# Kernel tuning notes

Measured on AMD Instinct MI355X. Metric: run time of the kernel, lower is better.

Reference implementation:

```python
import jax, jax.numpy as jnp
import numpy as np

N = 50000        # nodes
E = 800000       # directed edges (before self-loops)
F_IN = 128       # input node features
HID = 32         # hidden channels per head
HEADS = 4
NCLS = 8
EPS_BN = 1e-5
NEG_SLOPE = 0.2  # GATConv LeakyReLU default


def setup_inputs() -> dict:
    key = jax.random.key(0)
    ks = jax.random.split(key, 16)
    rn = lambda k, shape, s=0.1: jax.random.normal(k, shape, jnp.float32) * s
    inp = {}
    inp["x"] = jax.random.normal(ks[0], (N, F_IN), jnp.float32)
    inp["edge_index"] = jax.random.randint(ks[1], (2, E), 0, N, dtype=jnp.int32)
    # layer 0: F_IN -> HEADS*HID (concat)
    inp["W0"] = rn(ks[2], (F_IN, HEADS * HID))
    inp["as0"] = rn(ks[3], (HEADS, HID))
    inp["ad0"] = rn(ks[4], (HEADS, HID))
    inp["b0"] = jnp.zeros((HEADS * HID,), jnp.float32)
    inp["g0"] = jnp.ones((HEADS * HID,), jnp.float32)
    inp["bb0"] = jnp.zeros((HEADS * HID,), jnp.float32)
    inp["rm0"] = jnp.zeros((HEADS * HID,), jnp.float32)
    inp["rv0"] = jnp.ones((HEADS * HID,), jnp.float32)
    # layer 1: HEADS*HID -> HEADS*HID (concat)
    inp["W1"] = rn(ks[5], (HEADS * HID, HEADS * HID))
    inp["as1"] = rn(ks[6], (HEADS, HID))
    inp["ad1"] = rn(ks[7], (HEADS, HID))
    inp["b1"] = jnp.zeros((HEADS * HID,), jnp.float32)
    inp["g1"] = jnp.ones((HEADS * HID,), jnp.float32)
    inp["bb1"] = jnp.zeros((HEADS * HID,), jnp.float32)
    inp["rm1"] = jnp.zeros((HEADS * HID,), jnp.float32)
    inp["rv1"] = jnp.ones((HEADS * HID,), jnp.float32)
    # layer 2: HEADS*HID -> NCLS, heads=1, concat=False
    inp["W2"] = rn(ks[8], (HEADS * HID, NCLS))
    inp["as2"] = rn(ks[9], (1, NCLS))
    inp["ad2"] = rn(ks[10], (1, NCLS))
    inp["b2"] = jnp.zeros((NCLS,), jnp.float32)
    return inp


def gat_conv(x, src, dst, W, att_s, att_d, bias, H, C, concat):
    """PyG-style GATConv (eval mode, self-loops already appended to src/dst)."""
    n = x.shape[0]
    h = (x @ W).reshape(n, H, C)                       # [N,H,C]
    a_s = (h * att_s).sum(-1)                          # [N,H]
    a_d = (h * att_d).sum(-1)                          # [N,H]
    e = jax.nn.leaky_relu(a_s[src] + a_d[dst], NEG_SLOPE)  # [E,H]
    # numerically-stable segment softmax over incoming edges of each dst node
    m = jax.ops.segment_max(e, dst, num_segments=n)
    m = jnp.where(jnp.isfinite(m), m, 0.0)
    ex = jnp.exp(e - m[dst])
    den = jax.ops.segment_sum(ex, dst, num_segments=n)
    alpha = ex / (den[dst] + 1e-16)                    # [E,H]
    out = jax.ops.segment_sum(h[src] * alpha[:, :, None], dst, num_segments=n)  # [N,H,C]
    out = out.reshape(n, H * C) if concat else out.mean(axis=1)
    return out + bias


def bn_eval(x, g, b, rm, rv):
    return (x - rm) * jax.lax.rsqrt(rv + EPS_BN) * g + b


def reference(x, edge_index, W0, as0, ad0, b0, g0, bb0, rm0, rv0,
              W1, as1, ad1, b1, g1, bb1, rm1, rv1, W2, as2, ad2, b2):
    n = x.shape[0]
    loop = jnp.arange(n, dtype=edge_index.dtype)       # self-loops (PyG default)
    src = jnp.concatenate([edge_index[0], loop])
    dst = jnp.concatenate([edge_index[1], loop])
    h = gat_conv(x, src, dst, W0, as0, ad0, b0, HEADS, HID, True)
    h = jax.nn.elu(bn_eval(h, g0, bb0, rm0, rv0))
    h = gat_conv(h, src, dst, W1, as1, ad1, b1, HEADS, HID, True)
    h = jax.nn.elu(bn_eval(h, g1, bb1, rm1, rv1))
    h = gat_conv(h, src, dst, W2, as2, ad2, b2, 1, NCLS, False)
    return jax.nn.log_softmax(h, axis=1)
```

## Files before the change

kernel.cpp:

```cpp
#include <hip/hip_runtime.h>
#include <math.h>

#define N_NODES 50000
#define N_EDGES 800000
#define ET (N_EDGES + N_NODES)
#define FDIM 128
#define HEADS 4
#define HID 32
#define NCLS 8
#define NEG 0.2f
#define EPS_BN 1e-5f

#define BSH 6
#define NBUCK ((N_NODES + 63) >> BSH)
#define EPB 4096

typedef __attribute__((ext_vector_type(8))) short short8;
typedef __attribute__((ext_vector_type(4))) float f32x4;

__device__ __forceinline__ float lrelu(float e) { return e > 0.f ? e : NEG * e; }
__device__ __forceinline__ float bflo(unsigned u) { return __uint_as_float(u << 16); }
__device__ __forceinline__ float bfhi(unsigned u) { return __uint_as_float(u & 0xffff0000u); }
__device__ __forceinline__ unsigned f2bf(float f) {
    unsigned b = __float_as_uint(f);
    return (b + 0x7fffu + ((b >> 16) & 1u)) >> 16;
}

__device__ __forceinline__ void scan_bhist(const int* __restrict__ bhist,
                                           int* bloc, int* stmp) {
    int t = threadIdx.x;
    int idx = t * 4;
    int v0 = (idx     < NBUCK) ? bhist[idx]     : 0;
    int v1 = (idx + 1 < NBUCK) ? bhist[idx + 1] : 0;
    int v2 = (idx + 2 < NBUCK) ? bhist[idx + 2] : 0;
    int v3 = (idx + 3 < NBUCK) ? bhist[idx + 3] : 0;
    int sum = v0 + v1 + v2 + v3;
    stmp[t] = sum;
    __syncthreads();
    for (int off = 1; off < 256; off <<= 1) {
        int x = (t >= off) ? stmp[t - off] : 0;
        __syncthreads();
        stmp[t] += x;
        __syncthreads();
    }
    int run = stmp[t] - sum;
    if (idx     < NBUCK) bloc[idx]     = run; run += v0;
    if (idx + 1 < NBUCK) bloc[idx + 1] = run; run += v1;
    if (idx + 2 < NBUCK) bloc[idx + 2] = run; run += v2;
    if (idx + 3 < NBUCK) bloc[idx + 3] = run;
    __syncthreads();
}


#define CAST_B 3125
#define PACK_B 64
#define PB ((ET + EPB - 1) / EPB)

__global__ __launch_bounds__(256) void prep_hist(
        const float* __restrict__ x, unsigned short* __restrict__ xb,
        const float* __restrict__ W0, unsigned short* __restrict__ W0p,
        const float* __restrict__ W1, unsigned short* __restrict__ W1p,
        const int* __restrict__ ei, int* __restrict__ bhist) {
    __shared__ unsigned h[NBUCK];
    int b = blockIdx.x, tid = threadIdx.x;
    if (b < CAST_B) {
        int i = b * 256 + tid;
        const float4* p = (const float4*)x + (size_t)i * 2;
        float4 a = p[0], c = p[1];
        uint4 o;
        o.x = f2bf(a.x) | (f2bf(a.y) << 16);
        o.y = f2bf(a.z) | (f2bf(a.w) << 16);
        o.z = f2bf(c.x) | (f2bf(c.y) << 16);
        o.w = f2bf(c.z) | (f2bf(c.w) << 16);
        ((uint4*)xb)[i] = o;
    } else if (b < CAST_B + 2 * PACK_B) {
        int pb = b - CAST_B;
        const float* W = (pb < PACK_B) ? W0 : W1;
        unsigned short* Wp = (pb < PACK_B) ? W0p : W1p;
        int o = (pb & (PACK_B - 1)) * 256 + tid;
        int j = o & 7, lane = (o >> 3) & 63, kc = (o >> 9) & 3, t = o >> 11;
        int k = kc * 32 + ((lane >> 4) << 3) + j;
        int n = t * 16 + (lane & 15);
        Wp[o] = (unsigned short)f2bf(W[k * 128 + n]);
    } else {
        int blk = b - (CAST_B + 2 * PACK_B);
        int e0 = blk * EPB;
        for (int i = tid; i < NBUCK; i += 256) h[i] = 0;
        __syncthreads();
        #pragma unroll
        for (int k = 0; k < EPB / 256; k++) {
            int e = e0 + k * 256 + tid;
            if (e < ET) {
                int d = (e < N_EDGES) ? ei[N_EDGES + e] : (e - N_EDGES);
                atomicAdd(&h[d >> BSH], 1u);
            }
        }
        __syncthreads();
        for (int i = tid; i < NBUCK; i += 256)
            if (h[i]) atomicAdd(&bhist[i], (int)h[i]);
    }
}


__device__ __forceinline__ void gemm_attn_body(
        float* tiles, int gb,
        const unsigned short* __restrict__ Ab, const unsigned short* __restrict__ Wp,
        const float* __restrict__ att_s, const float* __restrict__ att_d,
        unsigned short* __restrict__ Hb, float* __restrict__ asn, float* __restrict__ adn,
        int M) {
    int tid = threadIdx.x;
    int wv = tid >> 6, lane = tid & 63;
    int base = gb * 64;
    int mrow = base + wv * 16 + (lane & 15);
    if (mrow >= M) mrow = M - 1;
    int koff = (lane >> 4) * 8;

    f32x4 acc[8];
    #pragma unroll
    for (int t = 0; t < 8; t++) acc[t] = (f32x4){0.f, 0.f, 0.f, 0.f};

    #pragma unroll
    for (int kc = 0; kc < 4; kc++) {
        short8 a = *(const short8*)(Ab + (size_t)mrow * 128 + kc * 32 + koff);
        #pragma unroll
        for (int t = 0; t < 8; t++) {
            short8 bfr = *(const short8*)(Wp + (((t * 4 + kc) * 64 + lane) << 3));
            acc[t] = __builtin_amdgcn_mfma_f32_16x16x32_bf16(a, bfr, acc[t], 0, 0, 0);
        }
    }

    int rbase = wv * 16 + (lane >> 4) * 4;
    int col = lane & 15;
    #pragma unroll
    for (int t = 0; t < 8; t++)
        #pragma unroll
        for (int r = 0; r < 4; r++)
            tiles[(rbase + r) * 132 + t * 16 + col] = acc[t][r];
    __syncthreads();

    #pragma unroll
    for (int it = 0; it < 4; it++) {
        int u = tid + it * 256;
        int rl = u >> 4, cg = u & 15;
        int row = base + rl;
        if (row < M) {
            const float* p = tiles + rl * 132 + cg * 8;
            float4 v0 = *(const float4*)(p);
            float4 v1 = *(const float4*)(p + 4);
            uint4 o;
            o.x = f2bf(v0.x) | (f2bf(v0.y) << 16);
            o.y = f2bf(v0.z) | (f2bf(v0.w) << 16);
            o.z = f2bf(v1.x) | (f2bf(v1.y) << 16);
            o.w = f2bf(v1.z) | (f2bf(v1.w) << 16);
            *(uint4*)(Hb + (size_t)row * 128 + cg * 8) = o;
        }
    }

    {
        int rl = tid >> 2, hd = tid & 3;
        int row = base + rl;
        if (row < M) {
            const float* hrow = tiles + rl * 132 + hd * 32;
            const float* as = att_s + hd * 32;
            const float* ad = att_d + hd * 32;
            float ps = 0.f, pd = 0.f;
            #pragma unroll
            for (int i = 0; i < 8; i++) {
                float4 hv = *(const float4*)(hrow + i * 4);
                float4 sv = *(const float4*)(as + i * 4);
                float4 dv = *(const float4*)(ad + i * 4);
                ps += hv.x * sv.x + hv.y * sv.y + hv.z * sv.z + hv.w * sv.w;
                pd += hv.x * dv.x + hv.y * dv.y + hv.z * dv.z + hv.w * dv.w;
            }
            asn[row * 4 + hd] = ps;
            adn[row * 4 + hd] = pd;
        }
    }
}


__global__ __launch_bounds__(256) void part_gemm(
        const int* __restrict__ ei, const int* __restrict__ bhist,
        int* __restrict__ bcur, int2* __restrict__ pairs,
        const unsigned short* __restrict__ Ab, const unsigned short* __restrict__ Wp,
        const float* __restrict__ att_s, const float* __restrict__ att_d,
        unsigned short* __restrict__ Hb, float* __restrict__ asn, float* __restrict__ adn,
        int M) {
    __shared__ float smem[64 * 132];
    int tid = threadIdx.x;
    if (blockIdx.x < PB) {
        unsigned* hist = (unsigned*)smem;
        unsigned* base = hist + NBUCK;
        int* bloc = (int*)(base + NBUCK);
        int* stmp = bloc + NBUCK;
        for (int i = tid; i < NBUCK; i += 256) hist[i] = 0;
        scan_bhist(bhist, bloc, stmp);
        int e0 = blockIdx.x * EPB;
        #pragma unroll
        for (int k = 0; k < EPB / 256; k++) {
            int e = e0 + k * 256 + tid;
            if (e < ET) {
                int d = (e < N_EDGES) ? ei[N_EDGES + e] : (e - N_EDGES);
                atomicAdd(&hist[d >> BSH], 1u);
            }
        }
        __syncthreads();
        for (int i = tid; i < NBUCK; i += 256) {
            unsigned h = hist[i];
            base[i] = h ? (unsigned)(bloc[i] + atomicAdd(&bcur[i], (int)h)) : 0u;
            hist[i] = 0;
        }
        __syncthreads();
        #pragma unroll
        for (int k = 0; k < EPB / 256; k++) {
            int e = e0 + k * 256 + tid;
            if (e < ET) {
                int s, d;
                if (e < N_EDGES) { s = ei[e]; d = ei[N_EDGES + e]; }
                else             { s = d = e - N_EDGES; }
                int bk = d >> BSH;
                unsigned lpos = atomicAdd(&hist[bk], 1u);
                pairs[base[bk] + lpos] = make_int2(s, d);
            }
        }
    } else {
        gemm_attn_body(smem, blockIdx.x - PB, Ab, Wp, att_s, att_d, Hb, asn, adn, M);
    }
}


__global__ __launch_bounds__(256) void group_bucket(const int2* __restrict__ pairs,
                                                    const int* __restrict__ bhist,
                                                    int* __restrict__ offs,
                                                    int* __restrict__ ssrc) {
    __shared__ int bloc[NBUCK];
    __shared__ int stmp[256];
    __shared__ int cnt[64];
    int b = blockIdx.x, tid = threadIdx.x;
    scan_bhist(bhist, bloc, stmp);
    int base = bloc[b];
    int end = (b + 1 < NBUCK) ? bloc[b + 1] : ET;
    int n0 = b << BSH;
    if (tid < 64) cnt[tid] = 0;
    __syncthreads();
    for (int i = base + tid; i < end; i += 256)
        atomicAdd(&cnt[pairs[i].y & 63], 1);
    __syncthreads();
    int v = (tid < 64) ? cnt[tid] : 0;
    stmp[tid] = v;
    __syncthreads();
    for (int off = 1; off < 64; off <<= 1) {
        int x = (tid >= off) ? stmp[tid - off] : 0;
        __syncthreads();
        stmp[tid] += x;
        __syncthreads();
    }
    int excl = stmp[tid] - v;
    if (tid < 64) {
        if (n0 + tid < N_NODES) offs[n0 + tid] = base + excl;
        cnt[tid] = excl;
    }
    __syncthreads();
    for (int i = base + tid; i < end; i += 256) {
        int2 p = pairs[i];
        int pos = atomicAdd(&cnt[p.y & 63], 1);
        ssrc[base + pos] = p.x;
    }
    if (b == 0 && tid == 0) offs[N_NODES] = ET;
}


#define AGB 16
#define NAGB (N_NODES / AGB)

__global__ __launch_bounds__(256) void agg_gemm1(
        const unsigned short* __restrict__ hb, const float* __restrict__ asn,
        const float* __restrict__ adn, const int* __restrict__ offs,
        const int* __restrict__ ssrc, const float* __restrict__ bias,
        const float* __restrict__ gamma, const float* __restrict__ beta,
        const float* __restrict__ rmean, const float* __restrict__ rvar,
        const unsigned short* __restrict__ Wp,
        const float* __restrict__ att_s, const float* __restrict__ att_d,
        unsigned short* __restrict__ Hb2, float* __restrict__ asn1,
        float* __restrict__ adn1) {
    __shared__ __attribute__((aligned(16))) unsigned short At[16][136];
    __shared__ __attribute__((aligned(16))) int2 sPair[4][4][72];
    float* ftile = (float*)&sPair[0][0][0];

    int tid = threadIdx.x;
    int wv = tid >> 6, lane = tid & 63;
    int hd = lane >> 4;
    const unsigned short* hlane = hb + 2 * lane;
    const int2* pp = &sPair[wv][hd][0];

    if (lane < 32) sPair[wv][lane >> 3][64 + (lane & 7)] = make_int2(0, 0);

    int c0 = lane * 2;
    float2 bi = *(const float2*)(bias + c0);
    float2 gm = *(const float2*)(gamma + c0);
    float2 bt = *(const float2*)(beta + c0);
    float2 rm = *(const float2*)(rmean + c0);
    float2 rv = *(const float2*)(rvar + c0);
    float sc0 = rsqrtf(rv.x + EPS_BN) * gm.x;
    float sc1 = rsqrtf(rv.y + EPS_BN) * gm.y;

    #pragma unroll 1
    for (int q = 0; q < 4; q++) {
        int lr = wv * 4 + q;
        int node = blockIdx.x * AGB + lr;
        int beg = offs[node], deg = offs[node + 1] - beg;
        float4 ad4 = *(const float4*)(adn + node * 4);
        float4 den4 = make_float4(0.f, 0.f, 0.f, 0.f);
        float acc0 = 0.f, acc1 = 0.f;

        auto phaseC = [&](int cnt) {
            int bound = (cnt + 7) & ~7;
            for (int i = 0; i < bound; i += 8) {
                int2 p0 = pp[i],     p1 = pp[i + 1], p2 = pp[i + 2], p3 = pp[i + 3];
                int2 p4 = pp[i + 4], p5 = pp[i + 5], p6 = pp[i + 6], p7 = pp[i + 7];
                unsigned u0 = *(const unsigned*)(hlane + (((unsigned)p0.x) << 7));
                unsigned u1 = *(const unsigned*)(hlane + (((unsigned)p1.x) << 7));
                unsigned u2 = *(const unsigned*)(hlane + (((unsigned)p2.x) << 7));
                unsigned u3 = *(const unsigned*)(hlane + (((unsigned)p3.x) << 7));
                unsigned u4 = *(const unsigned*)(hlane + (((unsigned)p4.x) << 7));
                unsigned u5 = *(const unsigned*)(hlane + (((unsigned)p5.x) << 7));
                unsigned u6 = *(const unsigned*)(hlane + (((unsigned)p6.x) << 7));
                unsigned u7 = *(const unsigned*)(hlane + (((unsigned)p7.x) << 7));
                acc0 += __int_as_float(p0.y) * bflo(u0); acc1 += __int_as_float(p0.y) * bfhi(u0);
                acc0 += __int_as_float(p1.y) * bflo(u1); acc1 += __int_as_float(p1.y) * bfhi(u1);
                acc0 += __int_as_float(p2.y) * bflo(u2); acc1 += __int_as_float(p2.y) * bfhi(u2);
                acc0 += __int_as_float(p3.y) * bflo(u3); acc1 += __int_as_float(p3.y) * bfhi(u3);
                acc0 += __int_as_float(p4.y) * bflo(u4); acc1 += __int_as_float(p4.y) * bfhi(u4);
                acc0 += __int_as_float(p5.y) * bflo(u5); acc1 += __int_as_float(p5.y) * bfhi(u5);
                acc0 += __int_as_float(p6.y) * bflo(u6); acc1 += __int_as_float(p6.y) * bfhi(u6);
                acc0 += __int_as_float(p7.y) * bflo(u7); acc1 += __int_as_float(p7.y) * bfhi(u7);
            }
        };

        for (int base0 = 0; base0 < deg; base0 += 64) {
            int j = base0 + lane;
            int s = 0;
            float4 w4 = make_float4(0.f, 0.f, 0.f, 0.f);
            if (j < deg) {
                s = ssrc[beg + j];
                float4 a = *(const float4*)(asn + s * 4);
                w4.x = __expf(lrelu(a.x + ad4.x));
                w4.y = __expf(lrelu(a.y + ad4.y));
                w4.z = __expf(lrelu(a.z + ad4.z));
                w4.w = __expf(lrelu(a.w + ad4.w));
                den4.x += w4.x; den4.y += w4.y; den4.z += w4.z; den4.w += w4.w;
            }
            sPair[wv][0][lane] = make_int2(s, __float_as_int(w4.x));
            sPair[wv][1][lane] = make_int2(s, __float_as_int(w4.y));
            sPair[wv][2][lane] = make_int2(s, __float_as_int(w4.z));
            sPair[wv][3][lane] = make_int2(s, __float_as_int(w4.w));
            int cnt = deg - base0; if (cnt > 64) cnt = 64;
            phaseC(cnt);
        }

        #pragma unroll
        for (int off = 32; off; off >>= 1) {
            den4.x += __shfl_xor(den4.x, off);
            den4.y += __shfl_xor(den4.y, off);
            den4.z += __shfl_xor(den4.z, off);
            den4.w += __shfl_xor(den4.w, off);
        }
        float den = (hd & 2) ? ((hd & 1) ? den4.w : den4.z)
                             : ((hd & 1) ? den4.y : den4.x);
        float inv = 1.f / (den + 1e-16f);

        float o0 = acc0 * inv + bi.x;
        float o1 = acc1 * inv + bi.y;
        o0 = (o0 - rm.x) * sc0 + bt.x;
        o1 = (o1 - rm.y) * sc1 + bt.y;
        o0 = (o0 > 0.f) ? o0 : expm1f(o0);
        o1 = (o1 > 0.f) ? o1 : expm1f(o1);
        *(unsigned*)&At[lr][c0] = f2bf(o0) | (f2bf(o1) << 16);
    }
    __syncthreads();

    int koff = hd * 8;
    int ar = lane & 15;
    f32x4 acc2[2];
    acc2[0] = (f32x4){0.f, 0.f, 0.f, 0.f};
    acc2[1] = (f32x4){0.f, 0.f, 0.f, 0.f};
    #pragma unroll
    for (int kc = 0; kc < 4; kc++) {
        short8 a = *(const short8*)&At[ar][kc * 32 + koff];
        #pragma unroll
        for (int ti = 0; ti < 2; ti++) {
            int t = wv * 2 + ti;
            short8 bfr = *(const short8*)(Wp + (((t * 4 + kc) * 64 + lane) << 3));
            acc2[ti] = __builtin_amdgcn_mfma_f32_16x16x32_bf16(a, bfr, acc2[ti], 0, 0, 0);
        }
    }
    __syncthreads();

    int rbase = hd * 4;
    int col = lane & 15;
    #pragma unroll
    for (int ti = 0; ti < 2; ti++) {
        int t = wv * 2 + ti;
        #pragma unroll
        for (int r = 0; r < 4; r++)
            ftile[(rbase + r) * 132 + t * 16 + col] = acc2[ti][r];
    }
    __syncthreads();

    {
        int rl = tid >> 4, cg = tid & 15;
        int row = blockIdx.x * AGB + rl;
        const float* p = ftile + rl * 132 + cg * 8;
        float4 v0 = *(const float4*)(p);
        float4 v1 = *(const float4*)(p + 4);
        uint4 o;
        o.x = f2bf(v0.x) | (f2bf(v0.y) << 16);
        o.y = f2bf(v0.z) | (f2bf(v0.w) << 16);
        o.z = f2bf(v1.x) | (f2bf(v1.y) << 16);
        o.w = f2bf(v1.z) | (f2bf(v1.w) << 16);
        *(uint4*)(Hb2 + (size_t)row * 128 + cg * 8) = o;
    }
    if (tid < 64) {
        int rl = tid >> 2, h2d = tid & 3;
        int row = blockIdx.x * AGB + rl;
        const float* hrow = ftile + rl * 132 + h2d * 32;
        const float* as = att_s + h2d * 32;
        const float* ad = att_d + h2d * 32;
        float ps = 0.f, pd = 0.f;
        #pragma unroll
        for (int i = 0; i < 8; i++) {
            float4 hv = *(const float4*)(hrow + i * 4);
            float4 sv = *(const float4*)(as + i * 4);
            float4 dv = *(const float4*)(ad + i * 4);
            ps += hv.x * sv.x + hv.y * sv.y + hv.z * sv.z + hv.w * sv.w;
            pd += hv.x * dv.x + hv.y * dv.y + hv.z * dv.z + hv.w * dv.w;
        }
        asn1[row * 4 + h2d] = ps;
        adn1[row * 4 + h2d] = pd;
    }
}


__global__ __launch_bounds__(256) void agg_mv2(
        const unsigned short* __restrict__ hb, const float* __restrict__ asn,
        const float* __restrict__ adn, const int* __restrict__ offs,
        const int* __restrict__ ssrc, const float* __restrict__ bias,
        const float* __restrict__ gamma, const float* __restrict__ beta,
        const float* __restrict__ rmean, const float* __restrict__ rvar,
        const float* __restrict__ W2, const float* __restrict__ as2,
        const float* __restrict__ ad2, float* __restrict__ h2,
        float* __restrict__ as2n, float* __restrict__ ad2n) {
    __shared__ int2 sPair[4][4][72];
    int wv = threadIdx.x >> 6;
    int node = blockIdx.x * 4 + wv;
    if (node >= N_NODES) return;
    int lane = threadIdx.x & 63;
    int hd = lane >> 4;
    int beg = offs[node], deg = offs[node + 1] - beg;
    float4 ad4 = *(const float4*)(adn + node * 4);

    if (lane < 32) sPair[wv][lane >> 3][64 + (lane & 7)] = make_int2(0, 0);

    float4 den4 = make_float4(0.f, 0.f, 0.f, 0.f);
    float acc0 = 0.f, acc1 = 0.f;
    const unsigned short* hlane = hb + 2 * lane;
    const int2* pp = &sPair[wv][hd][0];

    auto phaseC = [&](int cnt) {
        int bound = (cnt + 7) & ~7;
        for (int i = 0; i < bound; i += 8) {
            int2 p0 = pp[i],     p1 = pp[i + 1], p2 = pp[i + 2], p3 = pp[i + 3];
            int2 p4 = pp[i + 4], p5 = pp[i + 5], p6 = pp[i + 6], p7 = pp[i + 7];
            unsigned u0 = *(const unsigned*)(hlane + (((unsigned)p0.x) << 7));
            unsigned u1 = *(const unsigned*)(hlane + (((unsigned)p1.x) << 7));
            unsigned u2 = *(const unsigned*)(hlane + (((unsigned)p2.x) << 7));
            unsigned u3 = *(const unsigned*)(hlane + (((unsigned)p3.x) << 7));
            unsigned u4 = *(const unsigned*)(hlane + (((unsigned)p4.x) << 7));
            unsigned u5 = *(const unsigned*)(hlane + (((unsigned)p5.x) << 7));
            unsigned u6 = *(const unsigned*)(hlane + (((unsigned)p6.x) << 7));
            unsigned u7 = *(const unsigned*)(hlane + (((unsigned)p7.x) << 7));
            acc0 += __int_as_float(p0.y) * bflo(u0); acc1 += __int_as_float(p0.y) * bfhi(u0);
            acc0 += __int_as_float(p1.y) * bflo(u1); acc1 += __int_as_float(p1.y) * bfhi(u1);
            acc0 += __int_as_float(p2.y) * bflo(u2); acc1 += __int_as_float(p2.y) * bfhi(u2);
            acc0 += __int_as_float(p3.y) * bflo(u3); acc1 += __int_as_float(p3.y) * bfhi(u3);
            acc0 += __int_as_float(p4.y) * bflo(u4); acc1 += __int_as_float(p4.y) * bfhi(u4);
            acc0 += __int_as_float(p5.y) * bflo(u5); acc1 += __int_as_float(p5.y) * bfhi(u5);
            acc0 += __int_as_float(p6.y) * bflo(u6); acc1 += __int_as_float(p6.y) * bfhi(u6);
            acc0 += __int_as_float(p7.y) * bflo(u7); acc1 += __int_as_float(p7.y) * bfhi(u7);
        }
    };

    for (int base0 = 0; base0 < deg; base0 += 64) {
        int j = base0 + lane;
        int s = 0;
        float4 w4 = make_float4(0.f, 0.f, 0.f, 0.f);
        if (j < deg) {
            s = ssrc[beg + j];
            float4 a = *(const float4*)(asn + s * 4);
            w4.x = __expf(lrelu(a.x + ad4.x));
            w4.y = __expf(lrelu(a.y + ad4.y));
            w4.z = __expf(lrelu(a.z + ad4.z));
            w4.w = __expf(lrelu(a.w + ad4.w));
            den4.x += w4.x; den4.y += w4.y; den4.z += w4.z; den4.w += w4.w;
        }
        sPair[wv][0][lane] = make_int2(s, __float_as_int(w4.x));
        sPair[wv][1][lane] = make_int2(s, __float_as_int(w4.y));
        sPair[wv][2][lane] = make_int2(s, __float_as_int(w4.z));
        sPair[wv][3][lane] = make_int2(s, __float_as_int(w4.w));
        int cnt = deg - base0; if (cnt > 64) cnt = 64;
        phaseC(cnt);
    }

    #pragma unroll
    for (int off = 32; off; off >>= 1) {
        den4.x += __shfl_xor(den4.x, off);
        den4.y += __shfl_xor(den4.y, off);
        den4.z += __shfl_xor(den4.z, off);
        den4.w += __shfl_xor(den4.w, off);
    }
    float den = (hd & 2) ? ((hd & 1) ? den4.w : den4.z)
                         : ((hd & 1) ? den4.y : den4.x);
    float inv = 1.f / (den + 1e-16f);

    int c0 = lane * 2;
    float2 bi = *(const float2*)(bias + c0);
    float2 gm = *(const float2*)(gamma + c0);
    float2 bt = *(const float2*)(beta + c0);
    float2 rm = *(const float2*)(rmean + c0);
    float2 rv = *(const float2*)(rvar + c0);
    float o0 = acc0 * inv + bi.x;
    float o1 = acc1 * inv + bi.y;
    o0 = (o0 - rm.x) * rsqrtf(rv.x + EPS_BN) * gm.x + bt.x;
    o1 = (o1 - rm.y) * rsqrtf(rv.y + EPS_BN) * gm.y + bt.y;
    o0 = (o0 > 0.f) ? o0 : expm1f(o0);
    o1 = (o1 > 0.f) ? o1 : expm1f(o1);

    const float4* w2r = (const float4*)(W2 + c0 * 8);
    float4 wa0 = w2r[0], wa1 = w2r[1], wb0 = w2r[2], wb1 = w2r[3];
    float t8[8];
    t8[0] = o0 * wa0.x + o1 * wb0.x;
    t8[1] = o0 * wa0.y + o1 * wb0.y;
    t8[2] = o0 * wa0.z + o1 * wb0.z;
    t8[3] = o0 * wa0.w + o1 * wb0.w;
    t8[4] = o0 * wa1.x + o1 * wb1.x;
    t8[5] = o0 * wa1.y + o1 * wb1.y;
    t8[6] = o0 * wa1.z + o1 * wb1.z;
    t8[7] = o0 * wa1.w + o1 * wb1.w;
    #pragma unroll
    for (int off = 32; off; off >>= 1)
        #pragma unroll
        for (int c = 0; c < 8; c++) t8[c] += __shfl_xor(t8[c], off);
    if (lane == 0) {
        float ps = 0.f, pd = 0.f;
        #pragma unroll
        for (int c = 0; c < 8; c++) {
            h2[(size_t)node * 8 + c] = t8[c];
            ps += t8[c] * as2[c];
            pd += t8[c] * ad2[c];
        }
        as2n[node] = ps;
        ad2n[node] = pd;
    }
}


__global__ __launch_bounds__(256) void aggregate2(
        const float* __restrict__ h2, const float* __restrict__ asn,
        const float* __restrict__ adn, const int* __restrict__ offs,
        const int* __restrict__ ssrc, const float* __restrict__ b2,
        float* __restrict__ out) {
    __shared__ int2 sPair[4][64];
    int wv = threadIdx.x >> 6;
    int node = blockIdx.x * 4 + wv;
    if (node >= N_NODES) return;
    int lane = threadIdx.x & 63;
    int g = lane >> 3, c = lane & 7;
    int beg = offs[node], end = offs[node + 1];
    int deg = end - beg;
    float adv = adn[node];

    float den = 0.f, acc = 0.f;
    auto phaseC = [&](int cnt) {
        int nIt = (cnt + 15) >> 4;
        const int2* pp = &sPair[wv][0];
        for (int i = 0; i < nIt; i++) {
            int e = i * 16 + g;
            int2 p0 = pp[e];
            int2 p1 = pp[e + 8];
            acc += __int_as_float(p0.y) * h2[(((unsigned)p0.x) << 3) + c];
            acc += __int_as_float(p1.y) * h2[(((unsigned)p1.x) << 3) + c];
        }
    };

    for (int base = 0; base < deg; base += 64) {
        int j = base + lane;
        int s = 0; float w = 0.f;
        if (j < deg) {
            s = ssrc[beg + j];
            w = __expf(lrelu(asn[s] + adv));
            den += w;
        }
        sPair[wv][lane] = make_int2(s, __float_as_int(w));
        int cnt = deg - base; if (cnt > 64) cnt = 64;
        phaseC(cnt);
    }

    acc += __shfl_xor(acc, 8); acc += __shfl_xor(acc, 16); acc += __shfl_xor(acc, 32);
    #pragma unroll
    for (int off = 32; off; off >>= 1) den += __shfl_xor(den, off);

    float o = acc / (den + 1e-16f) + b2[c];
    float mx = o;
    mx = fmaxf(mx, __shfl_xor(mx, 1));
    mx = fmaxf(mx, __shfl_xor(mx, 2));
    mx = fmaxf(mx, __shfl_xor(mx, 4));
    float ex = __expf(o - mx);
    float sm = ex;
    sm += __shfl_xor(sm, 1); sm += __shfl_xor(sm, 2); sm += __shfl_xor(sm, 4);
    if (g == 0) out[(size_t)node * 8 + c] = o - mx - logf(sm);
}


extern "C" void kernel_launch(void* const* d_in, const int* in_sizes, int n_in,
                              void* d_out, int out_size, void* d_ws, size_t ws_size,
                              hipStream_t stream) {
    const float* x   = (const float*)d_in[0];
    const int*   ei  = (const int*)d_in[1];
    const float* W0  = (const float*)d_in[2];
    const float* as0 = (const float*)d_in[3];
    const float* ad0 = (const float*)d_in[4];
    const float* b0  = (const float*)d_in[5];
    const float* g0  = (const float*)d_in[6];
    const float* bb0 = (const float*)d_in[7];
    const float* rm0 = (const float*)d_in[8];
    const float* rv0 = (const float*)d_in[9];
    const float* W1  = (const float*)d_in[10];
    const float* as1 = (const float*)d_in[11];
    const float* ad1 = (const float*)d_in[12];
    const float* b1  = (const float*)d_in[13];
    const float* g1  = (const float*)d_in[14];
    const float* bb1 = (const float*)d_in[15];
    const float* rm1 = (const float*)d_in[16];
    const float* rv1 = (const float*)d_in[17];
    const float* W2  = (const float*)d_in[18];
    const float* as2 = (const float*)d_in[19];
    const float* ad2 = (const float*)d_in[20];
    const float* b2  = (const float*)d_in[21];
    float* out = (float*)d_out;

    char* w = (char*)d_ws;
    size_t off = 0;
    auto carve = [&](size_t bytes) {
        void* p = w + off;
        off += (bytes + 255) & ~(size_t)255;
        return p;
    };
    unsigned short* xb   = (unsigned short*)carve((size_t)N_NODES * 128 * 2);
    unsigned short* Hb   = (unsigned short*)carve((size_t)N_NODES * 128 * 2);
    unsigned short* Hb2  = (unsigned short*)carve((size_t)N_NODES * 128 * 2);
    unsigned short* W0p  = (unsigned short*)carve(16384 * 2);
    unsigned short* W1p  = (unsigned short*)carve(16384 * 2);
    int*   offs   = (int*)carve((size_t)(N_NODES + 1) * 4);
    int*   bhist  = (int*)carve((size_t)NBUCK * 2 * 4);
    int*   bcur   = bhist + NBUCK;
    int*   ssrc   = (int*)carve((size_t)ET * 4);
    int2*  pairs  = (int2*)carve((size_t)ET * 8);
    float* asn0   = (float*)carve((size_t)N_NODES * 4 * 4);
    float* adn0   = (float*)carve((size_t)N_NODES * 4 * 4);
    float* asn1   = (float*)carve((size_t)N_NODES * 4 * 4);
    float* adn1   = (float*)carve((size_t)N_NODES * 4 * 4);
    float* h2     = (float*)carve((size_t)N_NODES * 8 * 4);
    float* as2n   = (float*)carve((size_t)N_NODES * 4);
    float* ad2n   = (float*)carve((size_t)N_NODES * 4);
    (void)ws_size; (void)in_sizes; (void)n_in; (void)out_size;

    const int GB = (N_NODES + 63) / 64;

    hipMemsetAsync(bhist, 0, (size_t)NBUCK * 2 * 4, stream);
    prep_hist<<<CAST_B + 2 * PACK_B + PB, 256, 0, stream>>>(x, xb, W0, W0p, W1, W1p, ei, bhist);
    part_gemm<<<PB + GB, 256, 0, stream>>>(ei, bhist, bcur, pairs,
                                           xb, W0p, as0, ad0, Hb, asn0, adn0, N_NODES);
    group_bucket<<<NBUCK, 256, 0, stream>>>(pairs, bhist, offs, ssrc);
    agg_gemm1<<<NAGB, 256, 0, stream>>>(Hb, asn0, adn0, offs, ssrc,
                                        b0, g0, bb0, rm0, rv0,
                                        W1p, as1, ad1, Hb2, asn1, adn1);
    agg_mv2<<<(N_NODES + 3) / 4, 256, 0, stream>>>(Hb2, asn1, adn1, offs, ssrc,
                                                   b1, g1, bb1, rm1, rv1,
                                                   W2, as2, ad2, h2, as2n, ad2n);
    aggregate2<<<(N_NODES + 3) / 4, 256, 0, stream>>>(h2, as2n, ad2n, offs, ssrc, b2, out);
}
```

Before: 279.7 us.

## Vectorize edge gathers: 16-byte row loads with multiple edges per wavefront

The aggregation loops in agg_gemm1, agg_mv2 and aggregate2 are reorganized so each lane loads 16 bytes of a source row (8 bf16 or 4 floats) instead of 4 bytes. Several edges are now handled in parallel across lane groups, and partial sums are combined with cross-lane shuffles afterwards. This is meant to cut the number of gather instructions and serial iterations per edge on the memory-bound neighbour aggregation. In exchange it needs more accumulator registers and extra shuffle reductions, and in aggregate2 padded work grows for low-degree nodes because chunks are rounded up to 32.

```diff
diff --git a/kernel.cpp b/kernel.cpp
--- a/kernel.cpp
+++ b/kernel.cpp
@@ -289,20 +289,24 @@
 
     int tid = threadIdx.x;
     int wv = tid >> 6, lane = tid & 63;
-    int hd = lane >> 4;
-    const unsigned short* hlane = hb + 2 * lane;
-    const int2* pp = &sPair[wv][hd][0];
-
-    if (lane < 32) sPair[wv][lane >> 3][64 + (lane & 7)] = make_int2(0, 0);
-
-    int c0 = lane * 2;
-    float2 bi = *(const float2*)(bias + c0);
-    float2 gm = *(const float2*)(gamma + c0);
-    float2 bt = *(const float2*)(beta + c0);
-    float2 rm = *(const float2*)(rmean + c0);
-    float2 rv = *(const float2*)(rvar + c0);
-    float sc0 = rsqrtf(rv.x + EPS_BN) * gm.x;
-    float sc1 = rsqrtf(rv.y + EPS_BN) * gm.y;
+    int g = lane >> 4, sl = lane & 15;
+    int hda = sl >> 2;
+    const unsigned short* hsl = hb + (sl << 3);
+    const int2* pph = &sPair[wv][hda][0];
+    int c0 = sl * 8;
+
+    float4 bi0 = *(const float4*)(bias + c0),  bi1 = *(const float4*)(bias + c0 + 4);
+    float4 gm0 = *(const float4*)(gamma + c0), gm1 = *(const float4*)(gamma + c0 + 4);
+    float4 bt0 = *(const float4*)(beta + c0),  bt1 = *(const float4*)(beta + c0 + 4);
+    float4 rm0v = *(const float4*)(rmean + c0), rm1v = *(const float4*)(rmean + c0 + 4);
+    float4 rv0v = *(const float4*)(rvar + c0),  rv1v = *(const float4*)(rvar + c0 + 4);
+    float sc[8] = { rsqrtf(rv0v.x + EPS_BN) * gm0.x, rsqrtf(rv0v.y + EPS_BN) * gm0.y,
+                    rsqrtf(rv0v.z + EPS_BN) * gm0.z, rsqrtf(rv0v.w + EPS_BN) * gm0.w,
+                    rsqrtf(rv1v.x + EPS_BN) * gm1.x, rsqrtf(rv1v.y + EPS_BN) * gm1.y,
+                    rsqrtf(rv1v.z + EPS_BN) * gm1.z, rsqrtf(rv1v.w + EPS_BN) * gm1.w };
+    float bia[8] = { bi0.x, bi0.y, bi0.z, bi0.w, bi1.x, bi1.y, bi1.z, bi1.w };
+    float btv[8] = { bt0.x, bt0.y, bt0.z, bt0.w, bt1.x, bt1.y, bt1.z, bt1.w };
+    float rmv[8] = { rm0v.x, rm0v.y, rm0v.z, rm0v.w, rm1v.x, rm1v.y, rm1v.z, rm1v.w };
 
     #pragma unroll 1
     for (int q = 0; q < 4; q++) {
@@ -311,31 +315,7 @@
         int beg = offs[node], deg = offs[node + 1] - beg;
         float4 ad4 = *(const float4*)(adn + node * 4);
         float4 den4 = make_float4(0.f, 0.f, 0.f, 0.f);
-        float acc0 = 0.f, acc1 = 0.f;
-
-        auto phaseC = [&](int cnt) {
-            int bound = (cnt + 7) & ~7;
-            for (int i = 0; i < bound; i += 8) {
-                int2 p0 = pp[i],     p1 = pp[i + 1], p2 = pp[i + 2], p3 = pp[i + 3];
-                int2 p4 = pp[i + 4], p5 = pp[i + 5], p6 = pp[i + 6], p7 = pp[i + 7];
-                unsigned u0 = *(const unsigned*)(hlane + (((unsigned)p0.x) << 7));
-                unsigned u1 = *(const unsigned*)(hlane + (((unsigned)p1.x) << 7));
-                unsigned u2 = *(const unsigned*)(hlane + (((unsigned)p2.x) << 7));
-                unsigned u3 = *(const unsigned*)(hlane + (((unsigned)p3.x) << 7));
-                unsigned u4 = *(const unsigned*)(hlane + (((unsigned)p4.x) << 7));
-                unsigned u5 = *(const unsigned*)(hlane + (((unsigned)p5.x) << 7));
-                unsigned u6 = *(const unsigned*)(hlane + (((unsigned)p6.x) << 7));
-                unsigned u7 = *(const unsigned*)(hlane + (((unsigned)p7.x) << 7));
-                acc0 += __int_as_float(p0.y) * bflo(u0); acc1 += __int_as_float(p0.y) * bfhi(u0);
-                acc0 += __int_as_float(p1.y) * bflo(u1); acc1 += __int_as_float(p1.y) * bfhi(u1);
-                acc0 += __int_as_float(p2.y) * bflo(u2); acc1 += __int_as_float(p2.y) * bfhi(u2);
-                acc0 += __int_as_float(p3.y) * bflo(u3); acc1 += __int_as_float(p3.y) * bfhi(u3);
-                acc0 += __int_as_float(p4.y) * bflo(u4); acc1 += __int_as_float(p4.y) * bfhi(u4);
-                acc0 += __int_as_float(p5.y) * bflo(u5); acc1 += __int_as_float(p5.y) * bfhi(u5);
-                acc0 += __int_as_float(p6.y) * bflo(u6); acc1 += __int_as_float(p6.y) * bfhi(u6);
-                acc0 += __int_as_float(p7.y) * bflo(u7); acc1 += __int_as_float(p7.y) * bfhi(u7);
-            }
-        };
+        float acc[8] = {0.f, 0.f, 0.f, 0.f, 0.f, 0.f, 0.f, 0.f};
 
         for (int base0 = 0; base0 < deg; base0 += 64) {
             int j = base0 + lane;
@@ -355,9 +335,28 @@
             sPair[wv][2][lane] = make_int2(s, __float_as_int(w4.z));
             sPair[wv][3][lane] = make_int2(s, __float_as_int(w4.w));
             int cnt = deg - base0; if (cnt > 64) cnt = 64;
-            phaseC(cnt);
-        }
-
+            int bound = (cnt + 7) & ~7;
+            for (int i = 0; i < bound; i += 8) {
+                int2 pa = pph[i + g], pb = pph[i + 4 + g];
+                uint4 ua = *(const uint4*)(hsl + (((unsigned)pa.x) << 7));
+                uint4 ub = *(const uint4*)(hsl + (((unsigned)pb.x) << 7));
+                float wa = __int_as_float(pa.y), wb = __int_as_float(pb.y);
+                acc[0] += wa * bflo(ua.x); acc[1] += wa * bfhi(ua.x);
+                acc[2] += wa * bflo(ua.y); acc[3] += wa * bfhi(ua.y);
+                acc[4] += wa * bflo(ua.z); acc[5] += wa * bfhi(ua.z);
+                acc[6] += wa * bflo(ua.w); acc[7] += wa * bfhi(ua.w);
+                acc[0] += wb * bflo(ub.x); acc[1] += wb * bfhi(ub.x);
+                acc[2] += wb * bflo(ub.y); acc[3] += wb * bfhi(ub.y);
+                acc[4] += wb * bflo(ub.z); acc[5] += wb * bfhi(ub.z);
+                acc[6] += wb * bflo(ub.w); acc[7] += wb * bfhi(ub.w);
+            }
+        }
+
+        #pragma unroll
+        for (int c = 0; c < 8; c++) {
+            acc[c] += __shfl_xor(acc[c], 16);
+            acc[c] += __shfl_xor(acc[c], 32);
+        }
         #pragma unroll
         for (int off = 32; off; off >>= 1) {
             den4.x += __shfl_xor(den4.x, off);
@@ -365,21 +364,26 @@
             den4.z += __shfl_xor(den4.z, off);
             den4.w += __shfl_xor(den4.w, off);
         }
-        float den = (hd & 2) ? ((hd & 1) ? den4.w : den4.z)
-                             : ((hd & 1) ? den4.y : den4.x);
+        float den = (hda & 2) ? ((hda & 1) ? den4.w : den4.z)
+                              : ((hda & 1) ? den4.y : den4.x);
         float inv = 1.f / (den + 1e-16f);
 
-        float o0 = acc0 * inv + bi.x;
-        float o1 = acc1 * inv + bi.y;
-        o0 = (o0 - rm.x) * sc0 + bt.x;
-        o1 = (o1 - rm.y) * sc1 + bt.y;
-        o0 = (o0 > 0.f) ? o0 : expm1f(o0);
-        o1 = (o1 > 0.f) ? o1 : expm1f(o1);
-        *(unsigned*)&At[lr][c0] = f2bf(o0) | (f2bf(o1) << 16);
-    }
-    __syncthreads();
-
-    int koff = hd * 8;
+        unsigned dw[4];
+        #pragma unroll
+        for (int k = 0; k < 4; k++) {
+            float e0 = acc[2 * k] * inv + bia[2 * k];
+            float e1 = acc[2 * k + 1] * inv + bia[2 * k + 1];
+            e0 = (e0 - rmv[2 * k]) * sc[2 * k] + btv[2 * k];
+            e1 = (e1 - rmv[2 * k + 1]) * sc[2 * k + 1] + btv[2 * k + 1];
+            e0 = (e0 > 0.f) ? e0 : expm1f(e0);
+            e1 = (e1 > 0.f) ? e1 : expm1f(e1);
+            dw[k] = f2bf(e0) | (f2bf(e1) << 16);
+        }
+        if (g == 0) *(uint4*)&At[lr][c0] = make_uint4(dw[0], dw[1], dw[2], dw[3]);
+    }
+    __syncthreads();
+
+    int koff = (lane >> 4) * 8;
     int ar = lane & 15;
     f32x4 acc2[2];
     acc2[0] = (f32x4){0.f, 0.f, 0.f, 0.f};
@@ -396,7 +400,7 @@
     }
     __syncthreads();
 
-    int rbase = hd * 4;
+    int rbase = (lane >> 4) * 4;
     int col = lane & 15;
     #pragma unroll
     for (int ti = 0; ti < 2; ti++) {
@@ -455,40 +459,15 @@
     int node = blockIdx.x * 4 + wv;
     if (node >= N_NODES) return;
     int lane = threadIdx.x & 63;
-    int hd = lane >> 4;
+    int g = lane >> 4, sl = lane & 15;
+    int hda = sl >> 2;
     int beg = offs[node], deg = offs[node + 1] - beg;
     float4 ad4 = *(const float4*)(adn + node * 4);
 
-    if (lane < 32) sPair[wv][lane >> 3][64 + (lane & 7)] = make_int2(0, 0);
-
     float4 den4 = make_float4(0.f, 0.f, 0.f, 0.f);
-    float acc0 = 0.f, acc1 = 0.f;
-    const unsigned short* hlane = hb + 2 * lane;
-    const int2* pp = &sPair[wv][hd][0];
-
-    auto phaseC = [&](int cnt) {
-        int bound = (cnt + 7) & ~7;
-        for (int i = 0; i < bound; i += 8) {
-            int2 p0 = pp[i],     p1 = pp[i + 1], p2 = pp[i + 2], p3 = pp[i + 3];
-            int2 p4 = pp[i + 4], p5 = pp[i + 5], p6 = pp[i + 6], p7 = pp[i + 7];
-            unsigned u0 = *(const unsigned*)(hlane + (((unsigned)p0.x) << 7));
-            unsigned u1 = *(const unsigned*)(hlane + (((unsigned)p1.x) << 7));
-            unsigned u2 = *(const unsigned*)(hlane + (((unsigned)p2.x) << 7));
-            unsigned u3 = *(const unsigned*)(hlane + (((unsigned)p3.x) << 7));
-            unsigned u4 = *(const unsigned*)(hlane + (((unsigned)p4.x) << 7));
-            unsigned u5 = *(const unsigned*)(hlane + (((unsigned)p5.x) << 7));
-            unsigned u6 = *(const unsigned*)(hlane + (((unsigned)p6.x) << 7));
-            unsigned u7 = *(const unsigned*)(hlane + (((unsigned)p7.x) << 7));
-            acc0 += __int_as_float(p0.y) * bflo(u0); acc1 += __int_as_float(p0.y) * bfhi(u0);
-            acc0 += __int_as_float(p1.y) * bflo(u1); acc1 += __int_as_float(p1.y) * bfhi(u1);
-            acc0 += __int_as_float(p2.y) * bflo(u2); acc1 += __int_as_float(p2.y) * bfhi(u2);
-            acc0 += __int_as_float(p3.y) * bflo(u3); acc1 += __int_as_float(p3.y) * bfhi(u3);
-            acc0 += __int_as_float(p4.y) * bflo(u4); acc1 += __int_as_float(p4.y) * bfhi(u4);
-            acc0 += __int_as_float(p5.y) * bflo(u5); acc1 += __int_as_float(p5.y) * bfhi(u5);
-            acc0 += __int_as_float(p6.y) * bflo(u6); acc1 += __int_as_float(p6.y) * bfhi(u6);
-            acc0 += __int_as_float(p7.y) * bflo(u7); acc1 += __int_as_float(p7.y) * bfhi(u7);
-        }
-    };
+    float acc[8] = {0.f, 0.f, 0.f, 0.f, 0.f, 0.f, 0.f, 0.f};
+    const unsigned short* hsl = hb + (sl << 3);
+    const int2* pph = &sPair[wv][hda][0];
 
     for (int base0 = 0; base0 < deg; base0 += 64) {
         int j = base0 + lane;
@@ -508,9 +487,28 @@
         sPair[wv][2][lane] = make_int2(s, __float_as_int(w4.z));
         sPair[wv][3][lane] = make_int2(s, __float_as_int(w4.w));
         int cnt = deg - base0; if (cnt > 64) cnt = 64;
-        phaseC(cnt);
-    }
-
+        int bound = (cnt + 7) & ~7;
+        for (int i = 0; i < bound; i += 8) {
+            int2 pa = pph[i + g], pb = pph[i + 4 + g];
+            uint4 ua = *(const uint4*)(hsl + (((unsigned)pa.x) << 7));
+            uint4 ub = *(const uint4*)(hsl + (((unsigned)pb.x) << 7));
+            float wa = __int_as_float(pa.y), wb = __int_as_float(pb.y);
+            acc[0] += wa * bflo(ua.x); acc[1] += wa * bfhi(ua.x);
+            acc[2] += wa * bflo(ua.y); acc[3] += wa * bfhi(ua.y);
+            acc[4] += wa * bflo(ua.z); acc[5] += wa * bfhi(ua.z);
+            acc[6] += wa * bflo(ua.w); acc[7] += wa * bfhi(ua.w);
+            acc[0] += wb * bflo(ub.x); acc[1] += wb * bfhi(ub.x);
+            acc[2] += wb * bflo(ub.y); acc[3] += wb * bfhi(ub.y);
+            acc[4] += wb * bflo(ub.z); acc[5] += wb * bfhi(ub.z);
+            acc[6] += wb * bflo(ub.w); acc[7] += wb * bfhi(ub.w);
+        }
+    }
+
+    #pragma unroll
+    for (int c = 0; c < 8; c++) {
+        acc[c] += __shfl_xor(acc[c], 16);
+        acc[c] += __shfl_xor(acc[c], 32);
+    }
     #pragma unroll
     for (int off = 32; off; off >>= 1) {
         den4.x += __shfl_xor(den4.x, off);
@@ -518,38 +516,47 @@
         den4.z += __shfl_xor(den4.z, off);
         den4.w += __shfl_xor(den4.w, off);
     }
-    float den = (hd & 2) ? ((hd & 1) ? den4.w : den4.z)
-                         : ((hd & 1) ? den4.y : den4.x);
+    float den = (hda & 2) ? ((hda & 1) ? den4.w : den4.z)
+                          : ((hda & 1) ? den4.y : den4.x);
     float inv = 1.f / (den + 1e-16f);
 
-    int c0 = lane * 2;
-    float2 bi = *(const float2*)(bias + c0);
-    float2 gm = *(const float2*)(gamma + c0);
-    float2 bt = *(const float2*)(beta + c0);
-    float2 rm = *(const float2*)(rmean + c0);
-    float2 rv = *(const float2*)(rvar + c0);
-    float o0 = acc0 * inv + bi.x;
-    float o1 = acc1 * inv + bi.y;
-    o0 = (o0 - rm.x) * rsqrtf(rv.x + EPS_BN) * gm.x + bt.x;
-    o1 = (o1 - rm.y) * rsqrtf(rv.y + EPS_BN) * gm.y + bt.y;
-    o0 = (o0 > 0.f) ? o0 : expm1f(o0);
-    o1 = (o1 > 0.f) ? o1 : expm1f(o1);
-
-    const float4* w2r = (const float4*)(W2 + c0 * 8);
-    float4 wa0 = w2r[0], wa1 = w2r[1], wb0 = w2r[2], wb1 = w2r[3];
-    float t8[8];
-    t8[0] = o0 * wa0.x + o1 * wb0.x;
-    t8[1] = o0 * wa0.y + o1 * wb0.y;
-    t8[2] = o0 * wa0.z + o1 * wb0.z;
-    t8[3] = o0 * wa0.w + o1 * wb0.w;
-    t8[4] = o0 * wa1.x + o1 * wb1.x;
-    t8[5] = o0 * wa1.y + o1 * wb1.y;
-    t8[6] = o0 * wa1.z + o1 * wb1.z;
-    t8[7] = o0 * wa1.w + o1 * wb1.w;
-    #pragma unroll
-    for (int off = 32; off; off >>= 1)
-        #pragma unroll
-        for (int c = 0; c < 8; c++) t8[c] += __shfl_xor(t8[c], off);
+    int c0 = sl * 8;
+    float4 bi0 = *(const float4*)(bias + c0),  bi1 = *(const float4*)(bias + c0 + 4);
+    float4 gm0 = *(const float4*)(gamma + c0), gm1 = *(const float4*)(gamma + c0 + 4);
+    float4 bt0 = *(const float4*)(beta + c0),  bt1 = *(const float4*)(beta + c0 + 4);
+    float4 rm0v = *(const float4*)(rmean + c0), rm1v = *(const float4*)(rmean + c0 + 4);
+    float4 rv0v = *(const float4*)(rvar + c0),  rv1v = *(const float4*)(rvar + c0 + 4);
+    float bia[8] = { bi0.x, bi0.y, bi0.z, bi0.w, bi1.x, bi1.y, bi1.z, bi1.w };
+    float gmv[8] = { gm0.x, gm0.y, gm0.z, gm0.w, gm1.x, gm1.y, gm1.z, gm1.w };
+    float btv[8] = { bt0.x, bt0.y, bt0.z, bt0.w, bt1.x, bt1.y, bt1.z, bt1.w };
+    float rmv[8] = { rm0v.x, rm0v.y, rm0v.z, rm0v.w, rm1v.x, rm1v.y, rm1v.z, rm1v.w };
+    float rvv[8] = { rv0v.x, rv0v.y, rv0v.z, rv0v.w, rv1v.x, rv1v.y, rv1v.z, rv1v.w };
+
+    float o[8];
+    #pragma unroll
+    for (int k = 0; k < 8; k++) {
+        float e = acc[k] * inv + bia[k];
+        e = (e - rmv[k]) * rsqrtf(rvv[k] + EPS_BN) * gmv[k] + btv[k];
+        o[k] = (e > 0.f) ? e : expm1f(e);
+    }
+
+    float t8[8] = {0.f, 0.f, 0.f, 0.f, 0.f, 0.f, 0.f, 0.f};
+    #pragma unroll
+    for (int k = 0; k < 8; k++) {
+        const float4* wr = (const float4*)(W2 + (size_t)(c0 + k) * 8);
+        float4 wlo = wr[0], whi = wr[1];
+        t8[0] += o[k] * wlo.x; t8[1] += o[k] * wlo.y;
+        t8[2] += o[k] * wlo.z; t8[3] += o[k] * wlo.w;
+        t8[4] += o[k] * whi.x; t8[5] += o[k] * whi.y;
+        t8[6] += o[k] * whi.z; t8[7] += o[k] * whi.w;
+    }
+    #pragma unroll
+    for (int c = 0; c < 8; c++) {
+        t8[c] += __shfl_xor(t8[c], 1);
+        t8[c] += __shfl_xor(t8[c], 2);
+        t8[c] += __shfl_xor(t8[c], 4);
+        t8[c] += __shfl_xor(t8[c], 8);
+    }
     if (lane == 0) {
         float ps = 0.f, pd = 0.f;
         #pragma unroll
@@ -574,23 +581,14 @@
     int node = blockIdx.x * 4 + wv;
     if (node >= N_NODES) return;
     int lane = threadIdx.x & 63;
-    int g = lane >> 3, c = lane & 7;
-    int beg = offs[node], end = offs[node + 1];
-    int deg = end - beg;
+    int grp = lane >> 1, sub = lane & 1;
+    int beg = offs[node], deg = offs[node + 1] - beg;
     float adv = adn[node];
 
-    float den = 0.f, acc = 0.f;
-    auto phaseC = [&](int cnt) {
-        int nIt = (cnt + 15) >> 4;
-        const int2* pp = &sPair[wv][0];
-        for (int i = 0; i < nIt; i++) {
-            int e = i * 16 + g;
-            int2 p0 = pp[e];
-            int2 p1 = pp[e + 8];
-            acc += __int_as_float(p0.y) * h2[(((unsigned)p0.x) << 3) + c];
-            acc += __int_as_float(p1.y) * h2[(((unsigned)p1.x) << 3) + c];
-        }
-    };
+    float den = 0.f;
+    float acc[4] = {0.f, 0.f, 0.f, 0.f};
+    const int2* pp = &sPair[wv][0];
+    const float* hsub = h2 + (sub << 2);
 
     for (int base = 0; base < deg; base += 64) {
         int j = base + lane;
@@ -602,22 +600,42 @@
         }
         sPair[wv][lane] = make_int2(s, __float_as_int(w));
         int cnt = deg - base; if (cnt > 64) cnt = 64;
-        phaseC(cnt);
-    }
-
-    acc += __shfl_xor(acc, 8); acc += __shfl_xor(acc, 16); acc += __shfl_xor(acc, 32);
+        int bound = (cnt + 31) & ~31;
+        for (int i = 0; i < bound; i += 32) {
+            int2 pr = pp[i + grp];
+            float wgt = __int_as_float(pr.y);
+            float4 v = *(const float4*)(hsub + (((unsigned)pr.x) << 3));
+            acc[0] += wgt * v.x; acc[1] += wgt * v.y;
+            acc[2] += wgt * v.z; acc[3] += wgt * v.w;
+        }
+    }
+
+    #pragma unroll
+    for (int c = 0; c < 4; c++) {
+        acc[c] += __shfl_xor(acc[c], 2);
+        acc[c] += __shfl_xor(acc[c], 4);
+        acc[c] += __shfl_xor(acc[c], 8);
+        acc[c] += __shfl_xor(acc[c], 16);
+        acc[c] += __shfl_xor(acc[c], 32);
+    }
     #pragma unroll
     for (int off = 32; off; off >>= 1) den += __shfl_xor(den, off);
-
-    float o = acc / (den + 1e-16f) + b2[c];
-    float mx = o;
+    float inv = 1.f / (den + 1e-16f);
+
+    float4 bv = *(const float4*)(b2 + (sub << 2));
+    float o0 = acc[0] * inv + bv.x;
+    float o1 = acc[1] * inv + bv.y;
+    float o2 = acc[2] * inv + bv.z;
+    float o3 = acc[3] * inv + bv.w;
+    float mx = fmaxf(fmaxf(o0, o1), fmaxf(o2, o3));
     mx = fmaxf(mx, __shfl_xor(mx, 1));
-    mx = fmaxf(mx, __shfl_xor(mx, 2));
-    mx = fmaxf(mx, __shfl_xor(mx, 4));
-    float ex = __expf(o - mx);
-    float sm = ex;
-    sm += __shfl_xor(sm, 1); sm += __shfl_xor(sm, 2); sm += __shfl_xor(sm, 4);
-    if (g == 0) out[(size_t)node * 8 + c] = o - mx - logf(sm);
+    float sm = __expf(o0 - mx) + __expf(o1 - mx) + __expf(o2 - mx) + __expf(o3 - mx);
+    sm += __shfl_xor(sm, 1);
+    if (lane < 2) {
+        float ls = logf(sm);
+        float4 ov = make_float4(o0 - mx - ls, o1 - mx - ls, o2 - mx - ls, o3 - mx - ls);
+        *(float4*)(out + (size_t)node * 8 + (sub << 2)) = ov;
+    }
 }
 
 
```

After: 367.8 us. 31.5% more time.

## Precompute per-edge attention weights in separate edge-parallel passes

Applied to the files above, without the earlier changes.

Computes exp(leaky_relu(a_s[src]+a_d[dst])) per sorted edge in dedicated passes: fused into group_bucket for layer 0, and in new edge_w/edge_w2k kernels for layers 1 and 2. The aggregation kernels then read contiguous precomputed weights instead of gathering source attention scores and evaluating exp. The aim is to shorten latency-bound gathers inside the aggregation loop, at the cost of two extra kernel launches, an extra sorted-dst array, and writing and re-reading a per-edge weight buffer.

```diff
diff --git a/kernel.cpp b/kernel.cpp
--- a/kernel.cpp
+++ b/kernel.cpp
@@ -232,7 +232,11 @@
 __global__ __launch_bounds__(256) void group_bucket(const int2* __restrict__ pairs,
                                                     const int* __restrict__ bhist,
                                                     int* __restrict__ offs,
-                                                    int* __restrict__ ssrc) {
+                                                    int* __restrict__ ssrc,
+                                                    int* __restrict__ sdst,
+                                                    const float* __restrict__ asn0,
+                                                    const float* __restrict__ adn0,
+                                                    float* __restrict__ ew0) {
     __shared__ int bloc[NBUCK];
     __shared__ int stmp[256];
     __shared__ int cnt[64];
@@ -264,9 +268,46 @@
     for (int i = base + tid; i < end; i += 256) {
         int2 p = pairs[i];
         int pos = atomicAdd(&cnt[p.y & 63], 1);
-        ssrc[base + pos] = p.x;
+        int e = base + pos;
+        ssrc[e] = p.x;
+        sdst[e] = p.y;
+        float4 a = *(const float4*)(asn0 + p.x * 4);
+        float4 d = *(const float4*)(adn0 + p.y * 4);
+        float4 w;
+        w.x = __expf(lrelu(a.x + d.x));
+        w.y = __expf(lrelu(a.y + d.y));
+        w.z = __expf(lrelu(a.z + d.z));
+        w.w = __expf(lrelu(a.w + d.w));
+        *(float4*)(ew0 + (size_t)e * 4) = w;
     }
     if (b == 0 && tid == 0) offs[N_NODES] = ET;
+}
+
+
+__global__ __launch_bounds__(256) void edge_w(
+        const int* __restrict__ ssrc, const int* __restrict__ sdst,
+        const float* __restrict__ asn, const float* __restrict__ adn,
+        float* __restrict__ ew) {
+    int e = blockIdx.x * 256 + threadIdx.x;
+    if (e >= ET) return;
+    int s = ssrc[e], d = sdst[e];
+    float4 a = *(const float4*)(asn + s * 4);
+    float4 b = *(const float4*)(adn + d * 4);
+    float4 w;
+    w.x = __expf(lrelu(a.x + b.x));
+    w.y = __expf(lrelu(a.y + b.y));
+    w.z = __expf(lrelu(a.z + b.z));
+    w.w = __expf(lrelu(a.w + b.w));
+    *(float4*)(ew + (size_t)e * 4) = w;
+}
+
+__global__ __launch_bounds__(256) void edge_w2k(
+        const int* __restrict__ ssrc, const int* __restrict__ sdst,
+        const float* __restrict__ asn, const float* __restrict__ adn,
+        float* __restrict__ ew) {
+    int e = blockIdx.x * 256 + threadIdx.x;
+    if (e >= ET) return;
+    ew[e] = __expf(lrelu(asn[ssrc[e]] + adn[sdst[e]]));
 }
 
 
@@ -274,12 +315,11 @@
 #define NAGB (N_NODES / AGB)
 
 __global__ __launch_bounds__(256) void agg_gemm1(
-        const unsigned short* __restrict__ hb, const float* __restrict__ asn,
-        const float* __restrict__ adn, const int* __restrict__ offs,
-        const int* __restrict__ ssrc, const float* __restrict__ bias,
-        const float* __restrict__ gamma, const float* __restrict__ beta,
-        const float* __restrict__ rmean, const float* __restrict__ rvar,
-        const unsigned short* __restrict__ Wp,
+        const unsigned short* __restrict__ hb, const float* __restrict__ ew,
+        const int* __restrict__ offs, const int* __restrict__ ssrc,
+        const float* __restrict__ bias, const float* __restrict__ gamma,
+        const float* __restrict__ beta, const float* __restrict__ rmean,
+        const float* __restrict__ rvar, const unsigned short* __restrict__ Wp,
         const float* __restrict__ att_s, const float* __restrict__ att_d,
         unsigned short* __restrict__ Hb2, float* __restrict__ asn1,
         float* __restrict__ adn1) {
@@ -309,7 +349,6 @@
         int lr = wv * 4 + q;
         int node = blockIdx.x * AGB + lr;
         int beg = offs[node], deg = offs[node + 1] - beg;
-        float4 ad4 = *(const float4*)(adn + node * 4);
         float4 den4 = make_float4(0.f, 0.f, 0.f, 0.f);
         float acc0 = 0.f, acc1 = 0.f;
 
@@ -343,11 +382,7 @@
             float4 w4 = make_float4(0.f, 0.f, 0.f, 0.f);
             if (j < deg) {
                 s = ssrc[beg + j];
-                float4 a = *(const float4*)(asn + s * 4);
-                w4.x = __expf(lrelu(a.x + ad4.x));
-                w4.y = __expf(lrelu(a.y + ad4.y));
-                w4.z = __expf(lrelu(a.z + ad4.z));
-                w4.w = __expf(lrelu(a.w + ad4.w));
+                w4 = *(const float4*)(ew + (size_t)(beg + j) * 4);
                 den4.x += w4.x; den4.y += w4.y; den4.z += w4.z; den4.w += w4.w;
             }
             sPair[wv][0][lane] = make_int2(s, __float_as_int(w4.x));
@@ -442,14 +477,13 @@
 
 
 __global__ __launch_bounds__(256) void agg_mv2(
-        const unsigned short* __restrict__ hb, const float* __restrict__ asn,
-        const float* __restrict__ adn, const int* __restrict__ offs,
-        const int* __restrict__ ssrc, const float* __restrict__ bias,
-        const float* __restrict__ gamma, const float* __restrict__ beta,
-        const float* __restrict__ rmean, const float* __restrict__ rvar,
-        const float* __restrict__ W2, const float* __restrict__ as2,
-        const float* __restrict__ ad2, float* __restrict__ h2,
-        float* __restrict__ as2n, float* __restrict__ ad2n) {
+        const unsigned short* __restrict__ hb, const float* __restrict__ ew,
+        const int* __restrict__ offs, const int* __restrict__ ssrc,
+        const float* __restrict__ bias, const float* __restrict__ gamma,
+        const float* __restrict__ beta, const float* __restrict__ rmean,
+        const float* __restrict__ rvar, const float* __restrict__ W2,
+        const float* __restrict__ as2, const float* __restrict__ ad2,
+        float* __restrict__ h2, float* __restrict__ as2n, float* __restrict__ ad2n) {
     __shared__ int2 sPair[4][4][72];
     int wv = threadIdx.x >> 6;
     int node = blockIdx.x * 4 + wv;
@@ -457,7 +491,6 @@
     int lane = threadIdx.x & 63;
     int hd = lane >> 4;
     int beg = offs[node], deg = offs[node + 1] - beg;
-    float4 ad4 = *(const float4*)(adn + node * 4);
 
     if (lane < 32) sPair[wv][lane >> 3][64 + (lane & 7)] = make_int2(0, 0);
 
@@ -496,11 +529,7 @@
         float4 w4 = make_float4(0.f, 0.f, 0.f, 0.f);
         if (j < deg) {
             s = ssrc[beg + j];
-            float4 a = *(const float4*)(asn + s * 4);
-            w4.x = __expf(lrelu(a.x + ad4.x));
-            w4.y = __expf(lrelu(a.y + ad4.y));
-            w4.z = __expf(lrelu(a.z + ad4.z));
-            w4.w = __expf(lrelu(a.w + ad4.w));
+            w4 = *(const float4*)(ew + (size_t)(beg + j) * 4);
             den4.x += w4.x; den4.y += w4.y; den4.z += w4.z; den4.w += w4.w;
         }
         sPair[wv][0][lane] = make_int2(s, __float_as_int(w4.x));
@@ -565,10 +594,9 @@
 
 
 __global__ __launch_bounds__(256) void aggregate2(
-        const float* __restrict__ h2, const float* __restrict__ asn,
-        const float* __restrict__ adn, const int* __restrict__ offs,
-        const int* __restrict__ ssrc, const float* __restrict__ b2,
-        float* __restrict__ out) {
+        const float* __restrict__ h2, const float* __restrict__ ew2,
+        const int* __restrict__ offs, const int* __restrict__ ssrc,
+        const float* __restrict__ b2, float* __restrict__ out) {
     __shared__ int2 sPair[4][64];
     int wv = threadIdx.x >> 6;
     int node = blockIdx.x * 4 + wv;
@@ -577,7 +605,6 @@
     int g = lane >> 3, c = lane & 7;
     int beg = offs[node], end = offs[node + 1];
     int deg = end - beg;
-    float adv = adn[node];
 
     float den = 0.f, acc = 0.f;
     auto phaseC = [&](int cnt) {
@@ -597,7 +624,7 @@
         int s = 0; float w = 0.f;
         if (j < deg) {
             s = ssrc[beg + j];
-            w = __expf(lrelu(asn[s] + adv));
+            w = ew2[beg + j];
             den += w;
         }
         sPair[wv][lane] = make_int2(s, __float_as_int(w));
@@ -664,6 +691,8 @@
     int*   bhist  = (int*)carve((size_t)NBUCK * 2 * 4);
     int*   bcur   = bhist + NBUCK;
     int*   ssrc   = (int*)carve((size_t)ET * 4);
+    int*   sdst   = (int*)carve((size_t)ET * 4);
+    float* ewf    = (float*)carve((size_t)ET * 4 * 4);
     int2*  pairs  = (int2*)carve((size_t)ET * 8);
     float* asn0   = (float*)carve((size_t)N_NODES * 4 * 4);
     float* adn0   = (float*)carve((size_t)N_NODES * 4 * 4);
@@ -675,17 +704,21 @@
     (void)ws_size; (void)in_sizes; (void)n_in; (void)out_size;
 
     const int GB = (N_NODES + 63) / 64;
+    const int EB = (ET + 255) / 256;
 
     hipMemsetAsync(bhist, 0, (size_t)NBUCK * 2 * 4, stream);
     prep_hist<<<CAST_B + 2 * PACK_B + PB, 256, 0, stream>>>(x, xb, W0, W0p, W1, W1p, ei, bhist);
     part_gemm<<<PB + GB, 256, 0, stream>>>(ei, bhist, bcur, pairs,
                                            xb, W0p, as0, ad0, Hb, asn0, adn0, N_NODES);
-    group_bucket<<<NBUCK, 256, 0, stream>>>(pairs, bhist, offs, ssrc);
-    agg_gemm1<<<NAGB, 256, 0, stream>>>(Hb, asn0, adn0, offs, ssrc,
+    group_bucket<<<NBUCK, 256, 0, stream>>>(pairs, bhist, offs, ssrc, sdst,
+                                            asn0, adn0, ewf);
+    agg_gemm1<<<NAGB, 256, 0, stream>>>(Hb, ewf, offs, ssrc,
                                         b0, g0, bb0, rm0, rv0,
                                         W1p, as1, ad1, Hb2, asn1, adn1);
-    agg_mv2<<<(N_NODES + 3) / 4, 256, 0, stream>>>(Hb2, asn1, adn1, offs, ssrc,
+    edge_w<<<EB, 256, 0, stream>>>(ssrc, sdst, asn1, adn1, ewf);
+    agg_mv2<<<(N_NODES + 3) / 4, 256, 0, stream>>>(Hb2, ewf, offs, ssrc,
                                                    b1, g1, bb1, rm1, rv1,
                                                    W2, as2, ad2, h2, as2n, ad2n);
-    aggregate2<<<(N_NODES + 3) / 4, 256, 0, stream>>>(h2, as2n, ad2n, offs, ssrc, b2, out);
-}
+    edge_w2k<<<EB, 256, 0, stream>>>(ssrc, sdst, as2n, ad2n, ewf);
+    aggregate2<<<(N_NODES + 3) / 4, 256, 0, stream>>>(h2, ewf, offs, ssrc, b2, out);
+}
```

New measurement: 294.7 us. 1.05x slower.
